# Kernel tuning notes

Measured on AMD Instinct MI355X. Metric: run time of the kernel, lower is better.

The kernel has to match this reference:

```python
import jax, jax.numpy as jnp
import numpy as np

HIDDEN, KEY_DIM, VALUE_DIM = 1024, 1024, 1024
BATCH, SEQ = 8, 2048


def setup_inputs() -> dict:
    key = jax.random.key(0)
    ks = jax.random.split(key, 9)
    s = lambda fan_in: 1.0 / np.sqrt(fan_in)
    return {
        "y_all": jax.random.normal(ks[0], (BATCH, SEQ, HIDDEN), dtype=jnp.float32),
        # torch nn.Linear weights stored as (in, out) for x @ W + b
        "Wq": jax.random.uniform(ks[1], (HIDDEN, KEY_DIM), jnp.float32, -s(HIDDEN), s(HIDDEN)),
        "bq": jax.random.uniform(ks[2], (KEY_DIM,), jnp.float32, -s(HIDDEN), s(HIDDEN)),
        "Wk": jax.random.uniform(ks[3], (HIDDEN, KEY_DIM), jnp.float32, -s(HIDDEN), s(HIDDEN)),
        "bk": jax.random.uniform(ks[4], (KEY_DIM,), jnp.float32, -s(HIDDEN), s(HIDDEN)),
        "Wv": jax.random.uniform(ks[5], (HIDDEN, VALUE_DIM), jnp.float32, -s(HIDDEN), s(HIDDEN)),
        "bv": jax.random.uniform(ks[6], (VALUE_DIM,), jnp.float32, -s(HIDDEN), s(HIDDEN)),
        "Wo": jax.random.uniform(ks[7], (VALUE_DIM, HIDDEN), jnp.float32, -s(VALUE_DIM), s(VALUE_DIM)),
        "bo": jax.random.uniform(ks[8], (HIDDEN,), jnp.float32, -s(VALUE_DIM), s(VALUE_DIM)),
    }


def reference(y_all, Wq, bq, Wk, bk, Wv, bv, Wo, bo):
    # Original loops over t, each step attending last hidden state to the full
    # prefix. Equivalent to a single causal-masked attention pass.
    B, T, H = y_all.shape
    dk = Wq.shape[1]
    q = (y_all @ Wq + bq) / jnp.sqrt(jnp.asarray(dk, y_all.dtype))  # [B,T,dk]
    k = y_all @ Wk + bk                                              # [B,T,dk]
    v = y_all @ Wv + bv                                              # [B,T,dv]
    scores = jnp.einsum("bid,bjd->bij", q, k)                        # [B,T,T]
    causal = jnp.tril(jnp.ones((T, T), dtype=bool))                  # j <= i
    scores = jnp.where(causal, scores, -jnp.inf)
    weights = jax.nn.softmax(scores, axis=-1)
    ctx = jnp.einsum("bij,bjd->bid", weights, v)                     # [B,T,dv]
    return ctx @ Wo + bo                                             # [B,T,H]
```

## Files before the change

kernel.cpp:

```cpp
#include <hip/hip_runtime.h>

typedef __attribute__((ext_vector_type(8))) __bf16 bf16x8;
typedef __attribute__((ext_vector_type(4))) float f32x4;
typedef __attribute__((ext_vector_type(4))) float f4;
typedef __attribute__((ext_vector_type(4))) unsigned short ushort4_t;

__device__ inline void gload16(const void* g, void* l) {
  __builtin_amdgcn_global_load_lds(
      (const __attribute__((address_space(1))) unsigned int*)g,
      (__attribute__((address_space(3))) unsigned int*)l, 16, 0, 0);
}

__global__ void convert_bf16_k(const float* __restrict__ in, __bf16* __restrict__ out, int n8) {
  int i = blockIdx.x * blockDim.x + threadIdx.x;
  int stride = gridDim.x * blockDim.x;
  for (; i < n8; i += stride) {
    f4 a = ((const f4*)in)[2 * (long long)i];
    f4 b = ((const f4*)in)[2 * (long long)i + 1];
    bf16x8 o;
#pragma unroll
    for (int e = 0; e < 4; e++) { o[e] = (__bf16)a[e]; o[e + 4] = (__bf16)b[e]; }
    ((bf16x8*)out)[i] = o;
  }
}

__global__ void pack_bias_k(const float* __restrict__ bq, const float* __restrict__ bk,
                            const float* __restrict__ bv, float* __restrict__ out) {
  int i = blockIdx.x * 256 + threadIdx.x;
  if (i >= 3072) return;
  const float* src = (i < 1024) ? bq : (i < 2048) ? bk : bv;
  out[i] = src[i & 1023];
}

__global__ void transpose_w_k(const float* __restrict__ W0, const float* __restrict__ W1,
                              const float* __restrict__ W2, const float* __restrict__ W3,
                              __bf16* __restrict__ out) {
  int z = blockIdx.z;
  const float* W = (z == 0) ? W0 : (z == 1) ? W1 : (z == 2) ? W2 : W3;
  __bf16* O = out + (long long)z * 1048576;
  __shared__ float tile[32][33];
  int tx = threadIdx.x, ty = threadIdx.y;
  int n0 = blockIdx.x * 32, k0 = blockIdx.y * 32;
#pragma unroll
  for (int i = 0; i < 4; i++)
    tile[ty + i * 8][tx] = W[(long long)(k0 + ty + i * 8) * 1024 + n0 + tx];
  __syncthreads();
#pragma unroll
  for (int i = 0; i < 4; i++)
    O[(long long)(n0 + ty + i * 8) * 1024 + k0 + tx] = (__bf16)tile[tx][ty + i * 8];
}


#define ABUF(P, H) (lds + ((P) * 2 + (H)) * 8192)
#define BBUF(P, H) (lds + 32768 + ((P) * 2 + (H)) * 8192)

#define LOADA(P, MIB)                                                          \
  _Pragma("unroll") for (int mi = 0; mi < 4; mi++)                             \
      _Pragma("unroll") for (int kh = 0; kh < 2; kh++) {                       \
    int row = ((MIB) + mi) * 16 + ln15;                                        \
    int pb = (row * 128 + (kh * 32 + kq * 8) * 2) ^ ((row & 7) << 4);          \
    a[mi][kh] = *(const bf16x8*)((const char*)ABUF(P, wm) + pb);               \
  }

#define LOADB(P, NIB)                                                          \
  _Pragma("unroll") for (int ni = 0; ni < 2; ni++)                             \
      _Pragma("unroll") for (int kh = 0; kh < 2; kh++) {                       \
    int row = brow0 + ((NIB) + ni) * 16 + ln15;                                \
    int pb = (row * 128 + (kh * 32 + kq * 8) * 2) ^ ((row & 7) << 4);          \
    b[(NIB) + ni][kh] = *(const bf16x8*)((const char*)BBUF(P, bh) + pb);       \
  }

#define MFMAQ(MI0, NI0)                                                        \
  _Pragma("unroll") for (int mi = 0; mi < 4; mi++)                             \
      _Pragma("unroll") for (int ni = 0; ni < 2; ni++)                         \
          _Pragma("unroll") for (int kh = 0; kh < 2; kh++)                     \
              acc[(MI0) + mi][(NI0) + ni] =                                    \
      __builtin_amdgcn_mfma_f32_16x16x32_bf16(a[mi][kh], b[(NI0) + ni][kh],    \
                                              acc[(MI0) + mi][(NI0) + ni], 0, 0, 0);

#define FENCE asm volatile("" ::: "memory")

#define BARW                                           \
  FENCE;                                               \
  __builtin_amdgcn_s_barrier();                        \
  FENCE;                                               \
  __builtin_amdgcn_s_setprio(1);

#define ENDP                                           \
  __builtin_amdgcn_s_setprio(0);                       \
  FENCE;                                               \
  __builtin_amdgcn_s_barrier();                        \
  FENCE;

#define ENDPB                                          \
  __builtin_amdgcn_s_setprio(0);                       \
  asm volatile("s_waitcnt vmcnt(4)" ::: "memory");     \
  __builtin_amdgcn_s_barrier();                        \
  FENCE;

template <int OUT, int SWZ, int NSEG>
__global__ __launch_bounds__(512, 2) void gemm8(
    const __bf16* __restrict__ A0, int lda, long long sAz,
    const __bf16* __restrict__ B0, int ldb, long long sBz,
    void* __restrict__ C0v, int ldc, long long sCz,
    const float* __restrict__ bias0, int sBiasZ,
    float scale_z0, int k_tiles_base, int k_tiles_per_br,
    __bf16* __restrict__ vt_out) {
  int br, bc, z;
  {
    const int lin = (blockIdx.z * gridDim.y + blockIdx.y) * gridDim.x + blockIdx.x;
    if (SWZ == 1) {
      const int q = lin & 7, c = lin >> 3;
      br = q * 8 + (c & 7);
      bc = c >> 3;
      z = 0;
    } else if (SWZ == 2) {
      const int q = lin & 7, c = lin >> 3;
      z = q;
      int b0 = (int)((sqrtf((float)(8 * c + 1)) - 1.0f) * 0.5f);
      int c0 = c - ((b0 * (b0 + 1)) >> 1);
      if (c0 < 0) { b0--; c0 = c - ((b0 * (b0 + 1)) >> 1); }
      if (c0 > b0) { b0++; c0 = c - ((b0 * (b0 + 1)) >> 1); }
      br = b0;
      bc = c0;
    } else {
      const int nbx = gridDim.x, nby = gridDim.y;
      const int nwg = nbx * nby * gridDim.z;
      const int cpx = nwg >> 3;
      const int swz = (lin & 7) * cpx + (lin >> 3);
      br = swz % nbx;
      const int tmp = swz / nbx;
      bc = tmp % nby;
      z = tmp / nby;
    }
  }
  const int kt = k_tiles_base + k_tiles_per_br * br;
  const int ktend = kt * NSEG;

  __shared__ __align__(16) __bf16 lds[65536];

  const int t = threadIdx.x, w = t >> 6, lane = t & 63;
  const int wm = w >> 2, wn = w & 3;
  const int ln15 = lane & 15, kq = lane >> 4;
  const int bh = wn >> 1, brow0 = (wn & 1) * 64;

  const __bf16* A = A0 + (long long)z * sAz + (long long)br * 256 * lda;
  const __bf16* B = B0 + (long long)z * sBz + (long long)bc * 256 * ldb;
  if (SWZ == 1 && NSEG > 1) B = B0 + (long long)bc * 256 * ldb;

  int r0s[2], c0s[2];
#pragma unroll
  for (int i = 0; i < 2; i++) {
    int o = i * 8192 + t * 16;
    int lo = o ^ (((o >> 7) & 7) << 4);
    r0s[i] = lo >> 7;
    c0s[i] = (lo & 127) >> 1;
  }
  const __bf16 *sA0[2], *sA1[2], *sB0[2], *sB1[2];
#pragma unroll
  for (int i = 0; i < 2; i++) {
    sA0[i] = A + (long long)r0s[i] * lda + c0s[i];
    sA1[i] = A + (long long)(r0s[i] + 128) * lda + c0s[i];
    sB0[i] = B + (long long)r0s[i] * ldb + c0s[i];
    sB1[i] = B + (long long)(r0s[i] + 128) * ldb + c0s[i];
  }

  auto stg = [&](const __bf16* const* src, __bf16* lbase, int g, long long segstr) {
    int gc = g < ktend ? g : ktend - 1;
    int seg, kc;
    if (NSEG > 1) { seg = gc >> 4; kc = gc & 15; }
    else { seg = 0; kc = gc; }
#pragma unroll
    for (int i = 0; i < 2; i++)
      gload16(src[i] + (long long)seg * segstr + kc * 64, lbase + i * 4096 + w * 512);
  };

  f32x4 acc[8][4] = {};
  bf16x8 a[4][2], b[4][2];

  stg(sB0, BBUF(0, 0), 0, sBz);
  stg(sB1, BBUF(0, 1), 0, sBz);
  stg(sA0, ABUF(0, 0), 0, 0);
  stg(sA1, ABUF(0, 1), 0, 0);
  stg(sB0, BBUF(1, 0), 1, sBz);
  stg(sB1, BBUF(1, 1), 1, sBz);
  asm volatile("s_waitcnt vmcnt(4)" ::: "memory");
  __builtin_amdgcn_s_barrier();
  FENCE;

  for (int s = 0; s < NSEG; s++) {
    for (int kk = 0; kk < kt; kk += 2) {
      const int g = s * kt + kk;
      LOADA(0, 0) LOADB(0, 0)
      stg(sA0, ABUF(1, 0), g + 1, 0);
      BARW MFMAQ(0, 0) ENDP
      LOADB(0, 2)
      stg(sA1, ABUF(1, 1), g + 1, 0);
      BARW MFMAQ(0, 2) ENDP
      LOADA(0, 4)
      stg(sB0, BBUF(0, 0), g + 2, sBz);
      BARW MFMAQ(4, 2) ENDP
      stg(sB1, BBUF(0, 1), g + 2, sBz);
      BARW MFMAQ(4, 0) ENDPB
      LOADA(1, 0) LOADB(1, 0)
      stg(sA0, ABUF(0, 0), g + 2, 0);
      BARW MFMAQ(0, 0) ENDP
      LOADB(1, 2)
      stg(sA1, ABUF(0, 1), g + 2, 0);
      BARW MFMAQ(0, 2) ENDP
      LOADA(1, 4)
      stg(sB0, BBUF(1, 0), g + 3, sBz);
      BARW MFMAQ(4, 2) ENDP
      stg(sB1, BBUF(1, 1), g + 3, sBz);
      BARW MFMAQ(4, 0) ENDPB
    }
    if (OUT == 2 && s + 1 < NSEG) {
      const int ccb = (bc + 4 * s) * 256 + wn * 64 + ln15;
      const int rrb = br * 256 + wm * 128 + kq * 4;
      const float sc = (s == 0) ? scale_z0 : 1.0f;
#pragma unroll
      for (int mi = 0; mi < 8; mi++) {
#pragma unroll
        for (int ni = 0; ni < 4; ni++) {
          const int rr = rrb + mi * 16;
          const int cc = ccb + ni * 16;
          const float bb = bias0[cc];
#pragma unroll
          for (int j = 0; j < 4; j++)
            ((__bf16*)C0v)[(long long)(rr + j) * ldc + cc] =
                (__bf16)((acc[mi][ni][j] + bb) * sc);
          acc[mi][ni] = (f32x4){0.0f, 0.0f, 0.0f, 0.0f};
        }
      }
    }
  }

  if (OUT == 2) {
    __syncthreads();
    char* lb = (char*)lds;
    const int dl0 = wn * 64 + ln15;
    const int tl0 = wm * 128 + kq * 4;
#pragma unroll
    for (int mi = 0; mi < 8; mi++) {
#pragma unroll
      for (int ni = 0; ni < 4; ni++) {
        const int d = dl0 + ni * 16;
        const int tl = tl0 + mi * 16;
        const float bb = bias0[2048 + bc * 256 + d];
        ushort4_t p;
#pragma unroll
        for (int j = 0; j < 4; j++) {
          union { __bf16 h; unsigned short u; } cv;
          cv.h = (__bf16)(acc[mi][ni][j] + bb);
          p[j] = cv.u;
        }
        int byte = d * 512 + tl * 2;
        byte ^= (d & 7) << 4;
        *(ushort4_t*)(lb + byte) = p;
      }
    }
    __syncthreads();
    const int bz = br >> 3;
    __bf16* vbase = vt_out + (long long)bz * 2097152 +
                    (long long)(bc * 256) * 2048 + (br & 7) * 256;
#pragma unroll
    for (int it = 0; it < 16; it++) {
      int idx = it * 512 + t;
      int d = idx >> 5, tc = idx & 31;
      int byte = d * 512 + tc * 16;
      byte ^= (d & 7) << 4;
      bf16x8 vv = *(const bf16x8*)(lb + byte);
      *(bf16x8*)(vbase + (long long)d * 2048 + tc * 8) = vv;
    }
  } else {
    const int row0 = br * 256 + wm * 128 + kq * 4;
    const int col0 = bc * 256 + wn * 64 + ln15;
    const float scale = (z == 0) ? scale_z0 : 1.0f;
    const float* bias = bias0 ? (bias0 + (long long)z * sBiasZ) : nullptr;
#pragma unroll
    for (int mi = 0; mi < 8; mi++) {
#pragma unroll
      for (int ni = 0; ni < 4; ni++) {
        const int rr = row0 + mi * 16;
        const int cc = col0 + ni * 16;
        const float bb = bias ? bias[cc] : 0.0f;
#pragma unroll
        for (int j = 0; j < 4; j++) {
          float v = (acc[mi][ni][j] + bb) * scale;
          long long off = (long long)z * sCz + (long long)(rr + j) * ldc + cc;
          if (OUT == 1)
            ((float*)C0v)[off] = v;
          else
            ((__bf16*)C0v)[off] = (__bf16)v;
        }
      }
    }
  }
}

__global__ __launch_bounds__(256) void softmax_rows(__bf16* __restrict__ S) {
  const int row = blockIdx.x;
  const int i = row & 2047;
  __bf16* s = S + (long long)row * 2048;
  const int Lpad = (i + 256) & ~255;
  const int t = threadIdx.x;
  const int j0 = t * 8;
  const int wid = t >> 6, lane = t & 63;
  const bool active = j0 < Lpad;

  float v[8];
  float mymax = -3.0e38f;
  if (active) {
    bf16x8 x = *(const bf16x8*)(s + j0);
#pragma unroll
    for (int e = 0; e < 8; e++) {
      float f = (float)x[e];
      v[e] = ((j0 + e) <= i) ? f : -3.0e38f;
      mymax = fmaxf(mymax, v[e]);
    }
  }
  float mw = mymax;
#pragma unroll
  for (int o = 32; o >= 1; o >>= 1) mw = fmaxf(mw, __shfl_xor(mw, o));
  __shared__ float redm[4];
  __shared__ float reds[4];
  if (lane == 0) redm[wid] = mw;
  __syncthreads();
  const float m = fmaxf(fmaxf(redm[0], redm[1]), fmaxf(redm[2], redm[3]));

  float e8[8];
  float mysum = 0.0f;
  if (active) {
#pragma unroll
    for (int e = 0; e < 8; e++) {
      float ev = ((j0 + e) <= i) ? __expf(v[e] - m) : 0.0f;
      e8[e] = ev;
      mysum += ev;
    }
  } else {
#pragma unroll
    for (int e = 0; e < 8; e++) e8[e] = 0.0f;
  }
  float sw = mysum;
#pragma unroll
  for (int o = 32; o >= 1; o >>= 1) sw += __shfl_xor(sw, o);
  if (lane == 0) reds[wid] = sw;
  __syncthreads();
  const float l = reds[0] + reds[1] + reds[2] + reds[3];
  const float rl = 1.0f / l;
  if (active) {
    bf16x8 o;
#pragma unroll
    for (int e = 0; e < 8; e++) o[e] = (__bf16)(e8[e] * rl);
    *(bf16x8*)(s + j0) = o;
  }
}

extern "C" void kernel_launch(void* const* d_in, const int* in_sizes, int n_in,
                              void* d_out, int out_size, void* d_ws, size_t ws_size,
                              hipStream_t stream) {
  const float* y  = (const float*)d_in[0];
  const float* Wq = (const float*)d_in[1];
  const float* bq = (const float*)d_in[2];
  const float* Wk = (const float*)d_in[3];
  const float* bk = (const float*)d_in[4];
  const float* Wv = (const float*)d_in[5];
  const float* bv = (const float*)d_in[6];
  const float* Wo = (const float*)d_in[7];
  const float* bo = (const float*)d_in[8];

  char* ws = (char*)d_ws;
  __bf16* Xb   = (__bf16*)(ws + 0);
  __bf16* Wt   = (__bf16*)(ws + 33554432);
  float*  bqkv = (float*)(ws + 41943040);
  __bf16* QK   = (__bf16*)(ws + 41955328);
  __bf16* Vt   = (__bf16*)(ws + 109064192);
  __bf16* Sb   = (__bf16*)(ws + 142618624);
  __bf16* ctx  = (__bf16*)(ws + 0);

  if (ws_size < 209727488u) return;

  convert_bf16_k<<<2048, 256, 0, stream>>>(y, Xb, 2097152);
  pack_bias_k<<<12, 256, 0, stream>>>(bq, bk, bv, bqkv);
  transpose_w_k<<<dim3(32, 32, 4), dim3(32, 8), 0, stream>>>(Wq, Wk, Wv, Wo, Wt);

  gemm8<2, 1, 3><<<dim3(64, 4, 1), 512, 0, stream>>>(
      Xb, 1024, 0LL, Wt, 1024, 1048576LL,
      QK, 2048, 0LL, bqkv, 0, 0.03125f, 16, 0, Vt);

  gemm8<0, 2, 1><<<dim3(36, 1, 8), 512, 0, stream>>>(
      QK, 2048, 4194304LL, QK + 1024, 2048, 4194304LL,
      Sb, 2048, 4194304LL, nullptr, 0, 1.0f, 16, 0, nullptr);

  softmax_rows<<<16384, 256, 0, stream>>>(Sb);

  gemm8<0, 0, 1><<<dim3(8, 4, 8), 512, 0, stream>>>(
      Sb, 2048, 4194304LL, Vt, 2048, 2097152LL,
      ctx, 1024, 2097152LL, nullptr, 0, 1.0f, 4, 4, nullptr);

  gemm8<1, 1, 1><<<dim3(64, 4, 1), 512, 0, stream>>>(
      ctx, 1024, 0LL, Wt + 3 * 1048576, 1024, 0LL,
      d_out, 1024, 0LL, bo, 0, 1.0f, 16, 0, nullptr);
}
```

Before: 334.0 us.

## Triple-buffer A tiles in GEMM pipeline and split QKV projection across grid z

The GEMM main loop is rebuilt around a three-stage A buffer and two-stage B buffer. Each iteration now handles one k-tile and prefetches two tiles ahead, with the vmcnt wait raised to match, which needs more LDS. The fused multi-segment QKV projection (NSEG=3 looping in one block) becomes a 3-deep z grid writing separate Q and K buffers, with V transposed only at z==2. Block swizzles change as well, including a new batch-major mapping for the PV GEMM. This trades occupancy risk from the larger LDS footprint for deeper latency hiding and more parallel blocks in the projection.

```diff
diff --git a/kernel.cpp b/kernel.cpp
--- a/kernel.cpp
+++ b/kernel.cpp
@@ -51,23 +51,20 @@
 }
 
 
-#define ABUF(P, H) (lds + ((P) * 2 + (H)) * 8192)
-#define BBUF(P, H) (lds + 32768 + ((P) * 2 + (H)) * 8192)
-
-#define LOADA(P, MIB)                                                          \
+#define LOADA(BASE, MIB)                                                       \
   _Pragma("unroll") for (int mi = 0; mi < 4; mi++)                             \
       _Pragma("unroll") for (int kh = 0; kh < 2; kh++) {                       \
     int row = ((MIB) + mi) * 16 + ln15;                                        \
     int pb = (row * 128 + (kh * 32 + kq * 8) * 2) ^ ((row & 7) << 4);          \
-    a[mi][kh] = *(const bf16x8*)((const char*)ABUF(P, wm) + pb);               \
-  }
-
-#define LOADB(P, NIB)                                                          \
+    a[mi][kh] = *(const bf16x8*)((BASE) + pb);                                 \
+  }
+
+#define LOADB(BASE, NIB)                                                       \
   _Pragma("unroll") for (int ni = 0; ni < 2; ni++)                             \
       _Pragma("unroll") for (int kh = 0; kh < 2; kh++) {                       \
     int row = brow0 + ((NIB) + ni) * 16 + ln15;                                \
     int pb = (row * 128 + (kh * 32 + kq * 8) * 2) ^ ((row & 7) << 4);          \
-    b[(NIB) + ni][kh] = *(const bf16x8*)((const char*)BBUF(P, bh) + pb);       \
+    b[(NIB) + ni][kh] = *(const bf16x8*)((BASE) + pb);                         \
   }
 
 #define MFMAQ(MI0, NI0)                                                        \
@@ -94,11 +91,11 @@
 
 #define ENDPB                                          \
   __builtin_amdgcn_s_setprio(0);                       \
-  asm volatile("s_waitcnt vmcnt(4)" ::: "memory");     \
+  asm volatile("s_waitcnt vmcnt(8)" ::: "memory");     \
   __builtin_amdgcn_s_barrier();                        \
   FENCE;
 
-template <int OUT, int SWZ, int NSEG>
+template <int OUT, int SWZ>
 __global__ __launch_bounds__(512, 2) void gemm8(
     const __bf16* __restrict__ A0, int lda, long long sAz,
     const __bf16* __restrict__ B0, int ldb, long long sBz,
@@ -109,12 +106,7 @@
   int br, bc, z;
   {
     const int lin = (blockIdx.z * gridDim.y + blockIdx.y) * gridDim.x + blockIdx.x;
-    if (SWZ == 1) {
-      const int q = lin & 7, c = lin >> 3;
-      br = q * 8 + (c & 7);
-      bc = c >> 3;
-      z = 0;
-    } else if (SWZ == 2) {
+    if (SWZ == 2) {
       const int q = lin & 7, c = lin >> 3;
       z = q;
       int b0 = (int)((sqrtf((float)(8 * c + 1)) - 1.0f) * 0.5f);
@@ -123,6 +115,11 @@
       if (c0 > b0) { b0++; c0 = c - ((b0 * (b0 + 1)) >> 1); }
       br = b0;
       bc = c0;
+    } else if (SWZ == 3) {
+      const int q = lin & 7, c = lin >> 3;
+      z = q;
+      br = c & 7;
+      bc = c >> 3;
     } else {
       const int nbx = gridDim.x, nby = gridDim.y;
       const int nwg = nbx * nby * gridDim.z;
@@ -135,9 +132,8 @@
     }
   }
   const int kt = k_tiles_base + k_tiles_per_br * br;
-  const int ktend = kt * NSEG;
-
-  __shared__ __align__(16) __bf16 lds[65536];
+
+  __shared__ __align__(16) __bf16 lds[81920];
 
   const int t = threadIdx.x, w = t >> 6, lane = t & 63;
   const int wm = w >> 2, wn = w & 3;
@@ -146,7 +142,6 @@
 
   const __bf16* A = A0 + (long long)z * sAz + (long long)br * 256 * lda;
   const __bf16* B = B0 + (long long)z * sBz + (long long)bc * 256 * ldb;
-  if (SWZ == 1 && NSEG > 1) B = B0 + (long long)bc * 256 * ldb;
 
   int r0s[2], c0s[2];
 #pragma unroll
@@ -165,77 +160,53 @@
     sB1[i] = B + (long long)(r0s[i] + 128) * ldb + c0s[i];
   }
 
-  auto stg = [&](const __bf16* const* src, __bf16* lbase, int g, long long segstr) {
-    int gc = g < ktend ? g : ktend - 1;
-    int seg, kc;
-    if (NSEG > 1) { seg = gc >> 4; kc = gc & 15; }
-    else { seg = 0; kc = gc; }
+  auto stg = [&](const __bf16* const* src, __bf16* lbase, int g) {
+    int kc = g < kt ? g : kt - 1;
 #pragma unroll
     for (int i = 0; i < 2; i++)
-      gload16(src[i] + (long long)seg * segstr + kc * 64, lbase + i * 4096 + w * 512);
+      gload16(src[i] + kc * 64, lbase + i * 4096 + w * 512);
   };
 
   f32x4 acc[8][4] = {};
   bf16x8 a[4][2], b[4][2];
 
-  stg(sB0, BBUF(0, 0), 0, sBz);
-  stg(sB1, BBUF(0, 1), 0, sBz);
-  stg(sA0, ABUF(0, 0), 0, 0);
-  stg(sA1, ABUF(0, 1), 0, 0);
-  stg(sB0, BBUF(1, 0), 1, sBz);
-  stg(sB1, BBUF(1, 1), 1, sBz);
-  asm volatile("s_waitcnt vmcnt(4)" ::: "memory");
+  stg(sA0, lds, 0);
+  stg(sA1, lds + 8192, 0);
+  stg(sB0, lds + 49152, 0);
+  stg(sB1, lds + 49152 + 8192, 0);
+  stg(sA0, lds + 16384, 1);
+  stg(sA1, lds + 16384 + 8192, 1);
+  stg(sB0, lds + 65536, 1);
+  stg(sB1, lds + 65536 + 8192, 1);
+  asm volatile("s_waitcnt vmcnt(8)" ::: "memory");
   __builtin_amdgcn_s_barrier();
   FENCE;
 
-  for (int s = 0; s < NSEG; s++) {
-    for (int kk = 0; kk < kt; kk += 2) {
-      const int g = s * kt + kk;
-      LOADA(0, 0) LOADB(0, 0)
-      stg(sA0, ABUF(1, 0), g + 1, 0);
-      BARW MFMAQ(0, 0) ENDP
-      LOADB(0, 2)
-      stg(sA1, ABUF(1, 1), g + 1, 0);
-      BARW MFMAQ(0, 2) ENDP
-      LOADA(0, 4)
-      stg(sB0, BBUF(0, 0), g + 2, sBz);
-      BARW MFMAQ(4, 2) ENDP
-      stg(sB1, BBUF(0, 1), g + 2, sBz);
-      BARW MFMAQ(4, 0) ENDPB
-      LOADA(1, 0) LOADB(1, 0)
-      stg(sA0, ABUF(0, 0), g + 2, 0);
-      BARW MFMAQ(0, 0) ENDP
-      LOADB(1, 2)
-      stg(sA1, ABUF(0, 1), g + 2, 0);
-      BARW MFMAQ(0, 2) ENDP
-      LOADA(1, 4)
-      stg(sB0, BBUF(1, 0), g + 3, sBz);
-      BARW MFMAQ(4, 2) ENDP
-      stg(sB1, BBUF(1, 1), g + 3, sBz);
-      BARW MFMAQ(4, 0) ENDPB
-    }
-    if (OUT == 2 && s + 1 < NSEG) {
-      const int ccb = (bc + 4 * s) * 256 + wn * 64 + ln15;
-      const int rrb = br * 256 + wm * 128 + kq * 4;
-      const float sc = (s == 0) ? scale_z0 : 1.0f;
-#pragma unroll
-      for (int mi = 0; mi < 8; mi++) {
-#pragma unroll
-        for (int ni = 0; ni < 4; ni++) {
-          const int rr = rrb + mi * 16;
-          const int cc = ccb + ni * 16;
-          const float bb = bias0[cc];
-#pragma unroll
-          for (int j = 0; j < 4; j++)
-            ((__bf16*)C0v)[(long long)(rr + j) * ldc + cc] =
-                (__bf16)((acc[mi][ni][j] + bb) * sc);
-          acc[mi][ni] = (f32x4){0.0f, 0.0f, 0.0f, 0.0f};
-        }
-      }
-    }
-  }
-
-  if (OUT == 2) {
+  int ap = 0;
+  int ad = 2;
+  for (int kk = 0; kk < kt; kk++) {
+    __bf16* Ab = lds + ap * 16384;
+    __bf16* Bb = lds + 49152 + (kk & 1) * 16384;
+    __bf16* Ad = lds + ad * 16384;
+    __bf16* Bd = Bb;
+    const char* Aw = (const char*)(Ab + wm * 8192);
+    const char* Bw = (const char*)(Bb + bh * 8192);
+    LOADA(Aw, 0) LOADB(Bw, 0)
+    stg(sA0, Ad, kk + 2);
+    BARW MFMAQ(0, 0) ENDP
+    LOADB(Bw, 2)
+    stg(sA1, Ad + 8192, kk + 2);
+    BARW MFMAQ(0, 2) ENDP
+    LOADA(Aw, 4)
+    stg(sB0, Bd, kk + 2);
+    BARW MFMAQ(4, 2) ENDP
+    stg(sB1, Bd + 8192, kk + 2);
+    BARW MFMAQ(4, 0) ENDPB
+    ap = (ap == 2) ? 0 : ap + 1;
+    ad = (ad == 2) ? 0 : ad + 1;
+  }
+
+  if (OUT == 2 && z == 2) {
     __syncthreads();
     char* lb = (char*)lds;
     const int dl0 = wn * 64 + ln15;
@@ -373,7 +344,8 @@
   __bf16* Xb   = (__bf16*)(ws + 0);
   __bf16* Wt   = (__bf16*)(ws + 33554432);
   float*  bqkv = (float*)(ws + 41943040);
-  __bf16* QK   = (__bf16*)(ws + 41955328);
+  __bf16* Qb   = (__bf16*)(ws + 41955328);
+  __bf16* Kb   = (__bf16*)(ws + 75509760);
   __bf16* Vt   = (__bf16*)(ws + 109064192);
   __bf16* Sb   = (__bf16*)(ws + 142618624);
   __bf16* ctx  = (__bf16*)(ws + 0);
@@ -384,21 +356,21 @@
   pack_bias_k<<<12, 256, 0, stream>>>(bq, bk, bv, bqkv);
   transpose_w_k<<<dim3(32, 32, 4), dim3(32, 8), 0, stream>>>(Wq, Wk, Wv, Wo, Wt);
 
-  gemm8<2, 1, 3><<<dim3(64, 4, 1), 512, 0, stream>>>(
+  gemm8<2, 0><<<dim3(64, 4, 3), 512, 0, stream>>>(
       Xb, 1024, 0LL, Wt, 1024, 1048576LL,
-      QK, 2048, 0LL, bqkv, 0, 0.03125f, 16, 0, Vt);
-
-  gemm8<0, 2, 1><<<dim3(36, 1, 8), 512, 0, stream>>>(
-      QK, 2048, 4194304LL, QK + 1024, 2048, 4194304LL,
+      Qb, 1024, 16777216LL, bqkv, 1024, 0.03125f, 16, 0, Vt);
+
+  gemm8<0, 2><<<dim3(36, 1, 8), 512, 0, stream>>>(
+      Qb, 1024, 2097152LL, Kb, 1024, 2097152LL,
       Sb, 2048, 4194304LL, nullptr, 0, 1.0f, 16, 0, nullptr);
 
   softmax_rows<<<16384, 256, 0, stream>>>(Sb);
 
-  gemm8<0, 0, 1><<<dim3(8, 4, 8), 512, 0, stream>>>(
+  gemm8<0, 3><<<dim3(8, 4, 8), 512, 0, stream>>>(
       Sb, 2048, 4194304LL, Vt, 2048, 2097152LL,
       ctx, 1024, 2097152LL, nullptr, 0, 1.0f, 4, 4, nullptr);
 
-  gemm8<1, 1, 1><<<dim3(64, 4, 1), 512, 0, stream>>>(
+  gemm8<1, 0><<<dim3(64, 4, 1), 512, 0, stream>>>(
       ctx, 1024, 0LL, Wt + 3 * 1048576, 1024, 0LL,
       d_out, 1024, 0LL, bo, 0, 1.0f, 16, 0, nullptr);
 }
```

New measurement: 334.4 us. Within noise of the previous version (+0.1%).
